# Kernel optimization log

Measured on AMD Instinct MI355X. Metric: run time of the kernel, lower is better.

## Reference

```python
import jax, jax.numpy as jnp
import numpy as np

B, D, C, E, K = 4096, 784, 10, 1024, 8   # batch, input_size, num_classes, num_classifiers, k_neighbors
TANH_FACTOR = 10.0
EPS = 1e-12


def setup_inputs() -> dict:
    key = jax.random.key(0)
    ks = jax.random.split(key, 8)
    x = jax.random.normal(ks[0], (B, D), dtype=jnp.float32)
    keys_raw = jax.random.normal(ks[1], (E, D), dtype=jnp.float32)
    keys = keys_raw / jnp.maximum(jnp.linalg.norm(keys_raw, axis=1, keepdims=True), EPS)
    # weak-learner weights (VarianceScaling fan_in ~ 1/sqrt(D)) and biases
    Wm = jax.random.normal(ks[2], (E, C, D), dtype=jnp.float32) / jnp.sqrt(D)
    bm = jnp.zeros((E, C), dtype=jnp.float32)
    # vanilla classifier (scale=0.1 -> std ~ sqrt(0.1/D))
    Wv = jax.random.normal(ks[3], (C, D), dtype=jnp.float32) * jnp.sqrt(0.1 / D)
    bv = jnp.zeros((C,), dtype=jnp.float32)
    # tanh classifier
    Wt = jax.random.normal(ks[4], (C, D), dtype=jnp.float32) * jnp.sqrt(0.1 / D)
    bt = jnp.zeros((C,), dtype=jnp.float32)
    return {"x": x, "keys": keys, "Wm": Wm, "bm": bm, "Wv": Wv, "bv": bv, "Wt": Wt, "bt": bt}


def reference(x, keys, Wm, bm, Wv, bv, Wt, bt):
    # --- lookup_memory: cosine-similarity routing (keys are pre-normalized) ---
    xn = x / jnp.maximum(jnp.linalg.norm(x, axis=1, keepdims=True), EPS)  # l2 normalize
    cos = xn @ keys.T                       # [B, E]
    sims, idx = jax.lax.top_k(cos, K)       # descending similarity, [B, K]
    # Faithful to torch: experts are gathered in ascending model-index order
    # (enumerate over ModuleList), while weights `sims` stay similarity-sorted.
    gidx = jnp.sort(idx, axis=1)            # [B, K]

    # --- ensemble_forward: gather expert weights, per-sample tiny GEMVs ---
    Wg = Wm[gidx]                           # [B, K, C, D] (irregular gather)
    bg = bm[gidx]                           # [B, K, C]
    expert_raw = jnp.einsum('bd,bkcd->bkc', x, Wg) + bg
    expert_out = jnp.tanh(expert_raw / TANH_FACTOR) * TANH_FACTOR
    w = sims[..., None]                     # [B, K, 1]
    ensemble = jnp.sum(expert_out * w, axis=1) / jnp.sum(w, axis=1)  # [B, C]

    # --- vanilla / tanh classifiers ---
    vanilla = jax.nn.log_softmax(x @ Wv.T + bv, axis=1)
    tanh_out = jnp.tanh((x @ Wt.T + bt) / TANH_FACTOR) * TANH_FACTOR
    return ensemble, tanh_out, vanilla
```

## Files before the change

kernel.cpp:

```cpp
#include <hip/hip_runtime.h>
#include <hip/hip_bf16.h>
#include <math.h>

#define B_ 4096
#define D_ 784
#define C_ 10
#define E_ 1024
#define K_ 8
#define KP 832
#define CHR 104
#define NW 1088
#define LDR 72
#define LDW 840
#define CAP 48
#define ECAP 128

typedef float f32x4 __attribute__((ext_vector_type(4)));
typedef short s16x8 __attribute__((ext_vector_type(8)));

__device__ __forceinline__ float wave_reduce_sum(float v) {
  #pragma unroll
  for (int off = 32; off > 0; off >>= 1) v += __shfl_xor(v, off, 64);
  return v;
}

__global__ __launch_bounds__(256) void prep_all(const float* __restrict__ x,
                                                const float* __restrict__ keys,
                                                const float* __restrict__ Wv,
                                                const float* __restrict__ Wt,
                                                unsigned short* __restrict__ xh,
                                                unsigned short* __restrict__ kh,
                                                float* __restrict__ out_ens,
                                                int* __restrict__ count) {
  int gt = blockIdx.x * 256 + threadIdx.x;
  if (gt < E_) count[gt] = 0;
  int t = gt;
  const float* src = nullptr;
  unsigned short* dst;
  if (t < B_ * CHR) {
    int row = t / CHR, ch = t % CHR;
    dst = xh + (size_t)row * KP + ch * 8;
    src = (ch < 98) ? x + (size_t)row * D_ + ch * 8 : nullptr;
  } else {
    t -= B_ * CHR;
    if (t < NW * CHR) {
      int row = t / CHR, ch = t % CHR;
      dst = kh + (size_t)row * KP + ch * 8;
      if (ch < 98) {
        if (row < E_) src = keys + (size_t)row * D_ + ch * 8;
        else if (row < E_ + 10) src = Wv + (size_t)(row - E_) * D_ + ch * 8;
        else if (row < E_ + 20) src = Wt + (size_t)(row - E_ - 10) * D_ + ch * 8;
      }
    } else {
      t -= NW * CHR;
      if (t < (B_ * C_) / 4) {
        float4 z = make_float4(0.f, 0.f, 0.f, 0.f);
        ((float4*)out_ens)[t] = z;
      }
      return;
    }
  }
  unsigned short u[8];
  if (src) {
    #pragma unroll
    for (int i = 0; i < 8; ++i) {
      __hip_bfloat16 h = __float2bfloat16(src[i]);
      u[i] = *(unsigned short*)&h;
    }
  } else {
    #pragma unroll
    for (int i = 0; i < 8; ++i) u[i] = 0;
  }
  *(uint4*)dst = *(uint4*)u;
}

__global__ __launch_bounds__(256) void gemm_bf16(const unsigned short* __restrict__ xh,
                                                 const unsigned short* __restrict__ kh,
                                                 float* __restrict__ cosb) {
  __shared__ unsigned short As[64 * LDR];
  __shared__ unsigned short Bs[64 * LDR];
  const int tid  = threadIdx.x;
  const int row0 = blockIdx.y * 64, col0 = blockIdx.x * 64;
  const int srow = tid >> 2, sq = tid & 3;
  const int lane = tid & 63, w = tid >> 6;
  const int wr = (w >> 1) * 32, wc = (w & 1) * 32;
  const int fr = lane & 15, fg = lane >> 4;

  const unsigned short* gx = xh + (size_t)(row0 + srow) * KP;
  const unsigned short* gk = kh + (size_t)(col0 + srow) * KP;
  unsigned short* sa = As + srow * LDR + sq * 8;
  unsigned short* sb = Bs + srow * LDR + sq * 8;
  const unsigned short* pa0 = As + (wr + fr) * LDR + fg * 8;
  const unsigned short* pb0 = Bs + (wc + fr) * LDR + fg * 8;

  uint4 va0 = *(const uint4*)(gx + sq * 8);
  uint4 va1 = *(const uint4*)(gx + 32 + sq * 8);
  uint4 vb0 = *(const uint4*)(gk + sq * 8);
  uint4 vb1 = *(const uint4*)(gk + 32 + sq * 8);

  f32x4 acc[2][2] = {};
  for (int t = 0; t < 13; ++t) {
    __syncthreads();
    *(uint4*)sa = va0; *(uint4*)(sa + 32) = va1;
    *(uint4*)sb = vb0; *(uint4*)(sb + 32) = vb1;
    __syncthreads();
    if (t < 12) {
      int k1 = (t + 1) * 64;
      va0 = *(const uint4*)(gx + k1 + sq * 8);
      va1 = *(const uint4*)(gx + k1 + 32 + sq * 8);
      vb0 = *(const uint4*)(gk + k1 + sq * 8);
      vb1 = *(const uint4*)(gk + k1 + 32 + sq * 8);
    }
    #pragma unroll
    for (int kk = 0; kk < 64; kk += 32) {
      s16x8 a0 = *(const s16x8*)(pa0 + kk);
      s16x8 a1 = *(const s16x8*)(pa0 + 16 * LDR + kk);
      s16x8 b0 = *(const s16x8*)(pb0 + kk);
      s16x8 b1 = *(const s16x8*)(pb0 + 16 * LDR + kk);
      acc[0][0] = __builtin_amdgcn_mfma_f32_16x16x32_bf16(a0, b0, acc[0][0], 0, 0, 0);
      acc[0][1] = __builtin_amdgcn_mfma_f32_16x16x32_bf16(a0, b1, acc[0][1], 0, 0, 0);
      acc[1][0] = __builtin_amdgcn_mfma_f32_16x16x32_bf16(a1, b0, acc[1][0], 0, 0, 0);
      acc[1][1] = __builtin_amdgcn_mfma_f32_16x16x32_bf16(a1, b1, acc[1][1], 0, 0, 0);
    }
  }
  #pragma unroll
  for (int m = 0; m < 2; ++m)
    #pragma unroll
    for (int n = 0; n < 2; ++n)
      #pragma unroll
      for (int j = 0; j < 4; ++j) {
        int r = row0 + wr + m * 16 + fg * 4 + j;
        int c = col0 + wc + n * 16 + fr;
        cosb[(size_t)r * NW + c] = acc[m][n][j];
      }
}

__global__ __launch_bounds__(256) void topk_select(const float* __restrict__ cosb,
                                                   const float* __restrict__ x,
                                                   const float* __restrict__ keys,
                                                   const float* __restrict__ bv,
                                                   const float* __restrict__ bt,
                                                   float* __restrict__ sims,
                                                   int* __restrict__ count,
                                                   int* __restrict__ list,
                                                   float* __restrict__ out_tanh,
                                                   float* __restrict__ out_van) {
  __shared__ float sTop[32];
  __shared__ int   sIdx[CAP];
  __shared__ float sVal[CAP];
  __shared__ int   sCnt;
  __shared__ float sT8;
  const int tid = threadIdx.x, w = tid >> 6, lane = tid & 63;
  const int row = blockIdx.x;
  if (tid == 0) sCnt = 0;

  const float* cr = cosb + (size_t)row * NW;
  float vals[4];
  #pragma unroll
  for (int j = 0; j < 4; ++j) vals[j] = cr[j * 256 + tid];
  float lm = fmaxf(fmaxf(vals[0], vals[1]), fmaxf(vals[2], vals[3]));

  float v = lm;
  #pragma unroll
  for (int k = 2; k <= 64; k <<= 1) {
    #pragma unroll
    for (int j = k >> 1; j > 0; j >>= 1) {
      float o = __shfl_xor(v, j, 64);
      bool lower = (lane & j) == 0;
      bool asc = (lane & k) == 0;
      float mn = fminf(v, o), mx = fmaxf(v, o);
      v = (lower == asc) ? mn : mx;
    }
  }
  if (lane >= 56) sTop[w * 8 + (lane - 56)] = v;
  __syncthreads();

  if (w == 0) {
    float u = (lane < 32) ? sTop[lane] : -__builtin_inff();
    #pragma unroll
    for (int k = 2; k <= 64; k <<= 1) {
      #pragma unroll
      for (int j = k >> 1; j > 0; j >>= 1) {
        float o = __shfl_xor(u, j, 64);
        bool lower = (lane & j) == 0;
        bool asc = (lane & k) == 0;
        float mn = fminf(u, o), mx = fmaxf(u, o);
        u = (lower == asc) ? mn : mx;
      }
    }
    if (lane == 56) sT8 = u - 0.06f;
  }
  __syncthreads();
  const float t8 = sT8;

  #pragma unroll
  for (int j = 0; j < 4; ++j) {
    if (vals[j] >= t8) {
      int pos = atomicAdd(&sCnt, 1);
      if (pos < CAP) sIdx[pos] = j * 256 + tid;
    }
  }
  __syncthreads();
  const int m = sCnt < CAP ? sCnt : CAP;

  const float4* xp4 = (const float4*)(x + (size_t)row * D_);
  float4 xr[4];
  #pragma unroll
  for (int i = 0; i < 3; ++i) xr[i] = xp4[i * 64 + lane];
  xr[3] = make_float4(0.f, 0.f, 0.f, 0.f);
  if (lane < 4) xr[3] = xp4[192 + lane];
  float q = 0.f;
  #pragma unroll
  for (int i = 0; i < 4; ++i)
    q += xr[i].x * xr[i].x + xr[i].y * xr[i].y + xr[i].z * xr[i].z + xr[i].w * xr[i].w;
  q = wave_reduce_sum(q);
  const float rn = 1.0f / fmaxf(sqrtf(q), 1e-12f);

  for (int c = w; c < m; c += 4) {
    const float4* kp4 = (const float4*)(keys + (size_t)sIdx[c] * D_);
    float s = 0.f;
    #pragma unroll
    for (int i = 0; i < 3; ++i) {
      float4 kv = kp4[i * 64 + lane];
      s += xr[i].x * kv.x + xr[i].y * kv.y + xr[i].z * kv.z + xr[i].w * kv.w;
    }
    if (lane < 4) {
      float4 kv = kp4[192 + lane];
      s += xr[3].x * kv.x + xr[3].y * kv.y + xr[3].z * kv.z + xr[3].w * kv.w;
    }
    s = wave_reduce_sum(s);
    if (lane == 0) sVal[c] = s;
  }
  __syncthreads();

  if (w == 0) {
    unsigned long long key = 0;
    if (lane < m) {
      float ev = sVal[lane];
      int ei = sIdx[lane];
      unsigned ub = __float_as_uint(ev);
      ub = (ub & 0x80000000u) ? ~ub : (ub | 0x80000000u);
      key = ((unsigned long long)ub << 32) | (unsigned)(~ei);
    }
    #pragma unroll
    for (int k = 2; k <= 64; k <<= 1) {
      #pragma unroll
      for (int j = k >> 1; j > 0; j >>= 1) {
        unsigned long long o = __shfl_xor(key, j, 64);
        bool lower = (lane & j) == 0;
        bool asc = (lane & k) == 0;
        unsigned long long mn = key < o ? key : o;
        unsigned long long mx = key < o ? o : key;
        key = (lower == asc) ? mn : mx;
      }
    }
    if (lane >= 56) {
      unsigned ub = (unsigned)(key >> 32);
      unsigned fb = (ub & 0x80000000u) ? (ub ^ 0x80000000u) : ~ub;
      float ev = __uint_as_float(fb);
      int ei = (int)(~(unsigned)key) & (E_ - 1);
      float simv = ev * rn;
      float ssum = simv;
      ssum += __shfl_xor(ssum, 1, 64);
      ssum += __shfl_xor(ssum, 2, 64);
      ssum += __shfl_xor(ssum, 4, 64);
      int r = 63 - lane;
      sims[row * K_ + r] = simv / ssum;
      int si = ei;
      const int l3 = lane & 7;
      #pragma unroll
      for (int k = 2; k <= 8; k <<= 1) {
        #pragma unroll
        for (int j = k >> 1; j > 0; j >>= 1) {
          int o = __shfl_xor(si, j, 64);
          bool lower = (l3 & j) == 0;
          bool asc = (l3 & k) == 0;
          int mn = si < o ? si : o;
          int mx = si < o ? o : si;
          si = (lower == asc) ? mn : mx;
        }
      }
      int pos = atomicAdd(&count[si], 1);
      if (pos < ECAP) list[si * ECAP + pos] = row * K_ + (lane - 56);
    }
  } else if (w == 1) {
    float hv = (lane < 20) ? cr[E_ + lane] : 0.f;
    float vv = 0.f, tv = 0.f;
    if (lane < 10) vv = hv + bv[lane];
    else if (lane < 20) tv = hv + bt[lane - 10];
    float mv = (lane < 10) ? vv : -__builtin_inff();
    #pragma unroll
    for (int off = 1; off < 16; off <<= 1) mv = fmaxf(mv, __shfl_xor(mv, off, 64));
    float ev2 = (lane < 10) ? expf(vv - mv) : 0.f;
    float se = ev2;
    #pragma unroll
    for (int off = 1; off < 16; off <<= 1) se += __shfl_xor(se, off, 64);
    if (lane < 10) {
      out_van[(size_t)row * C_ + lane] = vv - (mv + logf(se));
    } else if (lane < 20) {
      out_tanh[(size_t)row * C_ + (lane - 10)] = tanhf(tv * 0.1f) * 10.0f;
    }
  }
}

__global__ __launch_bounds__(256) void expert_mfma(const float* __restrict__ Wm,
                                                   const float* __restrict__ bm,
                                                   const unsigned short* __restrict__ xh,
                                                   const int* __restrict__ list,
                                                   const int* __restrict__ count,
                                                   const float* __restrict__ sims,
                                                   float* __restrict__ out_ens) {
  __shared__ unsigned short Wl[16 * LDW];
  const int e   = blockIdx.x;
  const int tid = threadIdx.x;
  int n = count[e];
  n = n < ECAP ? n : ECAP;
  const int base = e * ECAP;

  for (int ch = tid; ch < 16 * CHR; ch += 256) {
    int r  = ch / CHR;
    int kc = (ch % CHR) * 8;
    unsigned short u[8];
    if (r < 10 && kc < 784) {
      const float* src = Wm + (size_t)e * (C_ * D_) + r * D_ + kc;
      #pragma unroll
      for (int i = 0; i < 8; ++i) {
        __hip_bfloat16 h = __float2bfloat16(src[i]);
        u[i] = *(unsigned short*)&h;
      }
    } else {
      #pragma unroll
      for (int i = 0; i < 8; ++i) u[i] = 0;
    }
    *(uint4*)(Wl + r * LDW + kc) = *(uint4*)u;
  }
  __syncthreads();
  if (n == 0) return;

  const int lane = tid & 63, w = tid >> 6;
  const int fr = lane & 15, fg = lane >> 4;
  const float bias = (fr < C_) ? bm[e * C_ + fr] : 0.f;
  const unsigned short* bp = Wl + fr * LDW + fg * 8;

  for (int c0 = w * 16; c0 < n; c0 += 64) {
    int sidx = c0 + fr;
    int item = (sidx < n) ? list[base + sidx] : list[base];
    const unsigned short* xrow = xh + (size_t)(item >> 3) * KP + fg * 8;
    f32x4 acc = {};
    #pragma unroll
    for (int k0 = 0; k0 < KP; k0 += 32) {
      s16x8 a = *(const s16x8*)(xrow + k0);
      s16x8 b = *(const s16x8*)(bp + k0);
      acc = __builtin_amdgcn_mfma_f32_16x16x32_bf16(a, b, acc, 0, 0, 0);
    }
    if (fr < C_) {
      #pragma unroll
      for (int j = 0; j < 4; ++j) {
        int s2 = c0 + fg * 4 + j;
        if (s2 < n) {
          int it2 = list[base + s2];
          float sc = sims[it2];
          float val = tanhf((acc[j] + bias) * 0.1f) * 10.0f;
          atomicAdd(&out_ens[(size_t)(it2 >> 3) * C_ + fr], val * sc);
        }
      }
    }
  }
}

extern "C" void kernel_launch(void* const* d_in, const int* in_sizes, int n_in,
                              void* d_out, int out_size, void* d_ws, size_t ws_size,
                              hipStream_t stream) {
  const float* x    = (const float*)d_in[0];
  const float* keys = (const float*)d_in[1];
  const float* Wm   = (const float*)d_in[2];
  const float* bm   = (const float*)d_in[3];
  const float* Wv   = (const float*)d_in[4];
  const float* bv   = (const float*)d_in[5];
  const float* Wt   = (const float*)d_in[6];
  const float* bt   = (const float*)d_in[7];
  float* out = (float*)d_out;
  float* out_ens  = out;
  float* out_tanh = out + (size_t)B_ * C_;
  float* out_van  = out + 2 * (size_t)B_ * C_;

  char* p = (char*)d_ws;
  auto carve = [&](size_t bytes) { char* q = p; p += (bytes + 255) & ~(size_t)255; return q; };
  float* cosb  = (float*)carve((size_t)B_ * NW * 4);
  float* sims  = (float*)carve(B_ * K_ * 4);
  unsigned short* xh = (unsigned short*)carve((size_t)B_ * KP * 2);
  unsigned short* kh = (unsigned short*)carve((size_t)NW * KP * 2);
  int*   count  = (int*)carve(E_ * 4);
  int*   list   = (int*)carve((size_t)E_ * ECAP * 4);

  int prep_threads = B_ * CHR + NW * CHR + (B_ * C_) / 4;
  prep_all<<<(prep_threads + 255) / 256, 256, 0, stream>>>(x, keys, Wv, Wt, xh, kh,
                                                           out_ens, count);
  dim3 g(NW / 64, B_ / 64);
  gemm_bf16<<<g, 256, 0, stream>>>(xh, kh, cosb);
  topk_select<<<B_, 256, 0, stream>>>(cosb, x, keys, bv, bt, sims, count, list,
                                      out_tanh, out_van);
  expert_mfma<<<E_, 256, 0, stream>>>(Wm, bm, xh, list, count, sims, out_ens);
}
```

Measured before the change: 86.57 us.

## Process one row per wave in top-k and rescore only ambiguous candidates in fp32

The top-k kernel now gives each row a single wavefront, so four rows share a block. Within a wave it collects candidates with ballot/popcount compaction, sorts the bf16 scores with a bitonic sort, and recomputes fp32 dot products only for candidates within a margin of the 8th score, and only when the 8th and 9th are close. The aim is to drop the block-wide syncs and the fp32 rescoring of every candidate. When no rescore happens, the returned sims are bf16-approximated scores, which is a correctness risk. The GEMM also gets a block-index swizzle for cache locality, and the expert weight load is vectorised to float4.

```diff
diff --git a/kernel.cpp b/kernel.cpp
--- a/kernel.cpp
+++ b/kernel.cpp
@@ -14,6 +14,7 @@
 #define LDW 840
 #define CAP 48
 #define ECAP 128
+#define MARG 0.04f
 
 typedef float f32x4 __attribute__((ext_vector_type(4)));
 typedef short s16x8 __attribute__((ext_vector_type(8)));
@@ -22,6 +23,41 @@
   #pragma unroll
   for (int off = 32; off > 0; off >>= 1) v += __shfl_xor(v, off, 64);
   return v;
+}
+
+__device__ __forceinline__ float bitonic64_f(float v, int lane) {
+  #pragma unroll
+  for (int k = 2; k <= 64; k <<= 1)
+    #pragma unroll
+    for (int j = k >> 1; j > 0; j >>= 1) {
+      float o = __shfl_xor(v, j, 64);
+      bool keepmin = ((lane & j) == 0) == ((lane & k) == 0);
+      v = keepmin ? fminf(v, o) : fmaxf(v, o);
+    }
+  return v;
+}
+
+__device__ __forceinline__ unsigned long long bitonic64_u(unsigned long long v, int lane) {
+  #pragma unroll
+  for (int k = 2; k <= 64; k <<= 1)
+    #pragma unroll
+    for (int j = k >> 1; j > 0; j >>= 1) {
+      unsigned long long o = __shfl_xor(v, j, 64);
+      bool keepmin = ((lane & j) == 0) == ((lane & k) == 0);
+      v = keepmin ? (v < o ? v : o) : (v < o ? o : v);
+    }
+  return v;
+}
+
+__device__ __forceinline__ unsigned long long packkey(float v, int idx) {
+  unsigned ub = __float_as_uint(v);
+  ub = (ub & 0x80000000u) ? ~ub : (ub | 0x80000000u);
+  return ((unsigned long long)ub << 32) | (unsigned)(~idx);
+}
+__device__ __forceinline__ float unpackval(unsigned long long k) {
+  unsigned ub = (unsigned)(k >> 32);
+  unsigned fb = (ub & 0x80000000u) ? (ub ^ 0x80000000u) : ~ub;
+  return __uint_as_float(fb);
 }
 
 __global__ __launch_bounds__(256) void prep_all(const float* __restrict__ x,
@@ -80,7 +116,9 @@
   __shared__ unsigned short As[64 * LDR];
   __shared__ unsigned short Bs[64 * LDR];
   const int tid  = threadIdx.x;
-  const int row0 = blockIdx.y * 64, col0 = blockIdx.x * 64;
+  const int bid  = blockIdx.y * 17 + blockIdx.x;
+  const int swz  = (bid & 7) * 136 + (bid >> 3);
+  const int row0 = (swz / 17) * 64, col0 = (swz % 17) * 64;
   const int srow = tid >> 2, sq = tid & 3;
   const int lane = tid & 63, w = tid >> 6;
   const int wr = (w >> 1) * 32, wc = (w & 1) * 32;
@@ -145,145 +183,12 @@
                                                    int* __restrict__ list,
                                                    float* __restrict__ out_tanh,
                                                    float* __restrict__ out_van) {
-  __shared__ float sTop[32];
-  __shared__ int   sIdx[CAP];
-  __shared__ float sVal[CAP];
-  __shared__ int   sCnt;
-  __shared__ float sT8;
+  __shared__ unsigned long long sKey[4][CAP];
   const int tid = threadIdx.x, w = tid >> 6, lane = tid & 63;
-  const int row = blockIdx.x;
-  if (tid == 0) sCnt = 0;
-
+  const int row = (blockIdx.x << 2) + w;
   const float* cr = cosb + (size_t)row * NW;
-  float vals[4];
-  #pragma unroll
-  for (int j = 0; j < 4; ++j) vals[j] = cr[j * 256 + tid];
-  float lm = fmaxf(fmaxf(vals[0], vals[1]), fmaxf(vals[2], vals[3]));
-
-  float v = lm;
-  #pragma unroll
-  for (int k = 2; k <= 64; k <<= 1) {
-    #pragma unroll
-    for (int j = k >> 1; j > 0; j >>= 1) {
-      float o = __shfl_xor(v, j, 64);
-      bool lower = (lane & j) == 0;
-      bool asc = (lane & k) == 0;
-      float mn = fminf(v, o), mx = fmaxf(v, o);
-      v = (lower == asc) ? mn : mx;
-    }
-  }
-  if (lane >= 56) sTop[w * 8 + (lane - 56)] = v;
-  __syncthreads();
-
-  if (w == 0) {
-    float u = (lane < 32) ? sTop[lane] : -__builtin_inff();
-    #pragma unroll
-    for (int k = 2; k <= 64; k <<= 1) {
-      #pragma unroll
-      for (int j = k >> 1; j > 0; j >>= 1) {
-        float o = __shfl_xor(u, j, 64);
-        bool lower = (lane & j) == 0;
-        bool asc = (lane & k) == 0;
-        float mn = fminf(u, o), mx = fmaxf(u, o);
-        u = (lower == asc) ? mn : mx;
-      }
-    }
-    if (lane == 56) sT8 = u - 0.06f;
-  }
-  __syncthreads();
-  const float t8 = sT8;
-
-  #pragma unroll
-  for (int j = 0; j < 4; ++j) {
-    if (vals[j] >= t8) {
-      int pos = atomicAdd(&sCnt, 1);
-      if (pos < CAP) sIdx[pos] = j * 256 + tid;
-    }
-  }
-  __syncthreads();
-  const int m = sCnt < CAP ? sCnt : CAP;
-
-  const float4* xp4 = (const float4*)(x + (size_t)row * D_);
-  float4 xr[4];
-  #pragma unroll
-  for (int i = 0; i < 3; ++i) xr[i] = xp4[i * 64 + lane];
-  xr[3] = make_float4(0.f, 0.f, 0.f, 0.f);
-  if (lane < 4) xr[3] = xp4[192 + lane];
-  float q = 0.f;
-  #pragma unroll
-  for (int i = 0; i < 4; ++i)
-    q += xr[i].x * xr[i].x + xr[i].y * xr[i].y + xr[i].z * xr[i].z + xr[i].w * xr[i].w;
-  q = wave_reduce_sum(q);
-  const float rn = 1.0f / fmaxf(sqrtf(q), 1e-12f);
-
-  for (int c = w; c < m; c += 4) {
-    const float4* kp4 = (const float4*)(keys + (size_t)sIdx[c] * D_);
-    float s = 0.f;
-    #pragma unroll
-    for (int i = 0; i < 3; ++i) {
-      float4 kv = kp4[i * 64 + lane];
-      s += xr[i].x * kv.x + xr[i].y * kv.y + xr[i].z * kv.z + xr[i].w * kv.w;
-    }
-    if (lane < 4) {
-      float4 kv = kp4[192 + lane];
-      s += xr[3].x * kv.x + xr[3].y * kv.y + xr[3].z * kv.z + xr[3].w * kv.w;
-    }
-    s = wave_reduce_sum(s);
-    if (lane == 0) sVal[c] = s;
-  }
-  __syncthreads();
-
-  if (w == 0) {
-    unsigned long long key = 0;
-    if (lane < m) {
-      float ev = sVal[lane];
-      int ei = sIdx[lane];
-      unsigned ub = __float_as_uint(ev);
-      ub = (ub & 0x80000000u) ? ~ub : (ub | 0x80000000u);
-      key = ((unsigned long long)ub << 32) | (unsigned)(~ei);
-    }
-    #pragma unroll
-    for (int k = 2; k <= 64; k <<= 1) {
-      #pragma unroll
-      for (int j = k >> 1; j > 0; j >>= 1) {
-        unsigned long long o = __shfl_xor(key, j, 64);
-        bool lower = (lane & j) == 0;
-        bool asc = (lane & k) == 0;
-        unsigned long long mn = key < o ? key : o;
-        unsigned long long mx = key < o ? o : key;
-        key = (lower == asc) ? mn : mx;
-      }
-    }
-    if (lane >= 56) {
-      unsigned ub = (unsigned)(key >> 32);
-      unsigned fb = (ub & 0x80000000u) ? (ub ^ 0x80000000u) : ~ub;
-      float ev = __uint_as_float(fb);
-      int ei = (int)(~(unsigned)key) & (E_ - 1);
-      float simv = ev * rn;
-      float ssum = simv;
-      ssum += __shfl_xor(ssum, 1, 64);
-      ssum += __shfl_xor(ssum, 2, 64);
-      ssum += __shfl_xor(ssum, 4, 64);
-      int r = 63 - lane;
-      sims[row * K_ + r] = simv / ssum;
-      int si = ei;
-      const int l3 = lane & 7;
-      #pragma unroll
-      for (int k = 2; k <= 8; k <<= 1) {
-        #pragma unroll
-        for (int j = k >> 1; j > 0; j >>= 1) {
-          int o = __shfl_xor(si, j, 64);
-          bool lower = (l3 & j) == 0;
-          bool asc = (l3 & k) == 0;
-          int mn = si < o ? si : o;
-          int mx = si < o ? o : si;
-          si = (lower == asc) ? mn : mx;
-        }
-      }
-      int pos = atomicAdd(&count[si], 1);
-      if (pos < ECAP) list[si * ECAP + pos] = row * K_ + (lane - 56);
-    }
-  } else if (w == 1) {
+
+  {
     float hv = (lane < 20) ? cr[E_ + lane] : 0.f;
     float vv = 0.f, tv = 0.f;
     if (lane < 10) vv = hv + bv[lane];
@@ -291,15 +196,99 @@
     float mv = (lane < 10) ? vv : -__builtin_inff();
     #pragma unroll
     for (int off = 1; off < 16; off <<= 1) mv = fmaxf(mv, __shfl_xor(mv, off, 64));
-    float ev2 = (lane < 10) ? expf(vv - mv) : 0.f;
-    float se = ev2;
+    float ev = (lane < 10) ? expf(vv - mv) : 0.f;
+    float se = ev;
     #pragma unroll
     for (int off = 1; off < 16; off <<= 1) se += __shfl_xor(se, off, 64);
-    if (lane < 10) {
-      out_van[(size_t)row * C_ + lane] = vv - (mv + logf(se));
-    } else if (lane < 20) {
-      out_tanh[(size_t)row * C_ + (lane - 10)] = tanhf(tv * 0.1f) * 10.0f;
-    }
+    if (lane < 10) out_van[(size_t)row * C_ + lane] = vv - (mv + logf(se));
+    else if (lane < 20) out_tanh[(size_t)row * C_ + (lane - 10)] = tanhf(tv * 0.1f) * 10.0f;
+  }
+
+  float vals[16];
+  #pragma unroll
+  for (int j = 0; j < 16; ++j) vals[j] = cr[j * 64 + lane];
+  float lm = vals[0];
+  #pragma unroll
+  for (int j = 1; j < 16; ++j) lm = fmaxf(lm, vals[j]);
+
+  float srt = bitonic64_f(lm, lane);
+  const float thr = __shfl(srt, 56) - MARG;
+
+  int cnt = 0;
+  #pragma unroll
+  for (int j = 0; j < 16; ++j) {
+    bool p = vals[j] >= thr;
+    unsigned long long mk = __ballot(p);
+    if (p) {
+      int pos = cnt + __popcll(mk & ((1ull << lane) - 1ull));
+      if (pos < CAP) sKey[w][pos] = packkey(vals[j], j * 64 + lane);
+    }
+    cnt += __popcll(mk);
+  }
+  const int m = cnt < CAP ? cnt : CAP;
+
+  unsigned long long key = (lane < m) ? sKey[w][lane] : 0ull;
+  key = bitonic64_u(key, lane);
+
+  const float a8 = unpackval(__shfl(key, 56));
+  const float a9 = unpackval(__shfl(key, 55));
+
+  if (a8 - a9 <= MARG) {
+    const float4* xp4 = (const float4*)(x + (size_t)row * D_);
+    float4 xr[4];
+    #pragma unroll
+    for (int i = 0; i < 3; ++i) xr[i] = xp4[i * 64 + lane];
+    xr[3] = make_float4(0.f, 0.f, 0.f, 0.f);
+    if (lane < 4) xr[3] = xp4[192 + lane];
+
+    float myv = unpackval(key);
+    unsigned long long rm = __ballot(key != 0ull && fabsf(myv - a8) <= MARG);
+    while (rm) {
+      int L = __builtin_ctzll(rm);
+      rm &= rm - 1;
+      unsigned long long kL = __shfl(key, L);
+      int ei = (int)(~(unsigned)kL) & (E_ - 1);
+      const float4* kp4 = (const float4*)(keys + (size_t)ei * D_);
+      float s = 0.f;
+      #pragma unroll
+      for (int i = 0; i < 3; ++i) {
+        float4 kv = kp4[i * 64 + lane];
+        s += xr[i].x * kv.x + xr[i].y * kv.y + xr[i].z * kv.z + xr[i].w * kv.w;
+      }
+      if (lane < 4) {
+        float4 kv = kp4[192 + lane];
+        s += xr[3].x * kv.x + xr[3].y * kv.y + xr[3].z * kv.z + xr[3].w * kv.w;
+      }
+      s = wave_reduce_sum(s);
+      if (lane == L) key = packkey(s, ei);
+    }
+    key = bitonic64_u(key, lane);
+  }
+
+  if (lane >= 56) {
+    float simv = unpackval(key);
+    int ei = (int)(~(unsigned)key) & (E_ - 1);
+    float ssum = simv;
+    ssum += __shfl_xor(ssum, 1, 64);
+    ssum += __shfl_xor(ssum, 2, 64);
+    ssum += __shfl_xor(ssum, 4, 64);
+    sims[row * K_ + (63 - lane)] = simv / ssum;
+    int si = ei;
+    const int l3 = lane & 7;
+    #pragma unroll
+    for (int k = 2; k <= 8; k <<= 1) {
+      #pragma unroll
+      for (int j = k >> 1; j > 0; j >>= 1) {
+        int o = __shfl_xor(si, j, 64);
+        bool lower = (l3 & j) == 0;
+        bool asc = (l3 & k) == 0;
+        int mn = si < o ? si : o;
+        int mx = si < o ? o : si;
+        si = (lower == asc) ? mn : mx;
+      }
+    }
+    int pos = atomicAdd(&count[si], 1);
+    if (pos < ECAP) list[si * ECAP + pos] = row * K_ + (lane - 56);
   }
 }
 
@@ -322,12 +311,17 @@
     int kc = (ch % CHR) * 8;
     unsigned short u[8];
     if (r < 10 && kc < 784) {
-      const float* src = Wm + (size_t)e * (C_ * D_) + r * D_ + kc;
-      #pragma unroll
-      for (int i = 0; i < 8; ++i) {
-        __hip_bfloat16 h = __float2bfloat16(src[i]);
-        u[i] = *(unsigned short*)&h;
-      }
+      const float4* s4 = (const float4*)(Wm + (size_t)e * (C_ * D_) + r * D_ + kc);
+      float4 f0 = s4[0], f1 = s4[1];
+      __hip_bfloat16 h;
+      h = __float2bfloat16(f0.x); u[0] = *(unsigned short*)&h;
+      h = __float2bfloat16(f0.y); u[1] = *(unsigned short*)&h;
+      h = __float2bfloat16(f0.z); u[2] = *(unsigned short*)&h;
+      h = __float2bfloat16(f0.w); u[3] = *(unsigned short*)&h;
+      h = __float2bfloat16(f1.x); u[4] = *(unsigned short*)&h;
+      h = __float2bfloat16(f1.y); u[5] = *(unsigned short*)&h;
+      h = __float2bfloat16(f1.z); u[6] = *(unsigned short*)&h;
+      h = __float2bfloat16(f1.w); u[7] = *(unsigned short*)&h;
     } else {
       #pragma unroll
       for (int i = 0; i < 8; ++i) u[i] = 0;
@@ -398,7 +392,7 @@
                                                            out_ens, count);
   dim3 g(NW / 64, B_ / 64);
   gemm_bf16<<<g, 256, 0, stream>>>(xh, kh, cosb);
-  topk_select<<<B_, 256, 0, stream>>>(cosb, x, keys, bv, bt, sims, count, list,
-                                      out_tanh, out_van);
+  topk_select<<<B_ / 4, 256, 0, stream>>>(cosb, x, keys, bv, bt, sims, count, list,
+                                          out_tanh, out_van);
   expert_mfma<<<E_, 256, 0, stream>>>(Wm, bm, xh, list, count, sims, out_ens);
 }
```

Result: faster. 80.72 us (-6.8%).
